# Performance work log

Hardware: AMD Instinct MI355X
Metric: run time of the kernel (lower is better)

## Reference

```python
import jax, jax.numpy as jnp
import numpy as np
from jax.ops import segment_sum, segment_max

DIM = 64; EDGE_DIM = 6; ACTION_DIM = 6
N = 16384; E = 32768; G = 256; TPG = 12  # nodes, edges, graphs, torsions/graph


def setup_inputs() -> dict:
    key = jax.random.key(0)
    ks = jax.random.split(key, 16)
    d = DIM
    def lin(k, fo, fi):
        return (jax.random.normal(k, (fo, fi), jnp.float32) / np.sqrt(fi)).astype(jnp.float32)
    return {
        "x": jax.random.normal(ks[0], (N, 3), jnp.float32),
        "edge_attr": jax.random.normal(ks[1], (E, EDGE_DIM), jnp.float32),
        "edge_index": jax.random.randint(ks[2], (2, E), 0, N),
        "batch": (jnp.arange(N) // (N // G)).astype(jnp.int32),
        "nonring": jax.random.randint(ks[3], (G * TPG, 4), 0, N),
        "nrbidx": (jnp.arange(G * TPG) // TPG).astype(jnp.int32),
        "num_graphs": G,
        "torsion_size": TPG,
        "lin0_w": lin(ks[4], d, 3), "lin0_b": jnp.zeros((d,), jnp.float32),
        "e1_w": lin(ks[5], d, EDGE_DIM), "e1_b": jnp.zeros((d,), jnp.float32),
        "e2_w": lin(ks[6], d * d, d), "e2_b": jnp.zeros((d * d,), jnp.float32),
        "root_w": lin(ks[7], d, d), "conv_b": jnp.zeros((d,), jnp.float32),
        "gru_wih": lin(ks[8], 3 * d, d), "gru_whh": lin(ks[9], 3 * d, d),
        "gru_bih": jnp.zeros((3 * d,), jnp.float32), "gru_bhh": jnp.zeros((3 * d,), jnp.float32),
        "s2s_wih": lin(ks[10], 4 * d, 2 * d), "s2s_whh": lin(ks[11], 4 * d, d),
        "s2s_bih": jnp.zeros((4 * d,), jnp.float32), "s2s_bhh": jnp.zeros((4 * d,), jnp.float32),
        "mem_wih": lin(ks[12], 4 * d, 2 * d), "mem_whh": lin(ks[13], 4 * d, d),
        "mem_bih": jnp.zeros((4 * d,), jnp.float32), "mem_bhh": jnp.zeros((4 * d,), jnp.float32),
        "lin1_w": lin(ks[14], d, 5 * d), "lin1_b": jnp.zeros((d,), jnp.float32),
        "lin2_w": lin(ks[15], ACTION_DIM, d), "lin2_b": jnp.zeros((ACTION_DIM,), jnp.float32),
    }


def _lstm_step(xin, h, c, wih, whh, bih, bhh):
    g = xin @ wih.T + bih + h @ whh.T + bhh
    i, f, gg, o = jnp.split(g, 4, axis=-1)
    c = jax.nn.sigmoid(f) * c + jax.nn.sigmoid(i) * jnp.tanh(gg)
    h = jax.nn.sigmoid(o) * jnp.tanh(c)
    return h, c


def _model(x, edge_attr, lin0_w, lin0_b, e1_w, e1_b, e2_w, e2_b, root_w, conv_b,
           gru_wih, gru_whh, gru_bih, gru_bhh, s2s_wih, s2s_whh, s2s_bih, s2s_bhh,
           mem_wih, mem_whh, mem_bih, mem_bhh, lin1_w, lin1_b, lin2_w, lin2_b,
           edge_index, batch, nonring, nrbidx, num_graphs, torsion_size):
    d = lin0_w.shape[0]
    n = x.shape[0]
    out = jax.nn.relu(x @ lin0_w.T + lin0_b)           # [N, d]
    h = out                                            # GRU hidden
    src, dst = edge_index[0], edge_index[1]
    # edge-conditioned weights (fixed across the 6 iterations -> computed once)
    ew = (jax.nn.relu(edge_attr @ e1_w.T + e1_b) @ e2_w.T + e2_b).reshape(-1, d, d)  # [E, d, d]
    deg = jnp.clip(segment_sum(jnp.ones((src.shape[0],), out.dtype), dst, num_segments=n), 1.0)
    for _ in range(6):
        msg = jnp.einsum('ei,eio->eo', out[src], ew)   # per-edge matmul, [E, d]
        agg = segment_sum(msg, dst, num_segments=n) / deg[:, None]  # scatter-mean
        m = jax.nn.relu(agg + out @ root_w + conv_b)
        gi = m @ gru_wih.T + gru_bih
        gh = h @ gru_whh.T + gru_bhh
        r = jax.nn.sigmoid(gi[:, :d] + gh[:, :d])
        z = jax.nn.sigmoid(gi[:, d:2 * d] + gh[:, d:2 * d])
        nnew = jnp.tanh(gi[:, 2 * d:] + r * gh[:, 2 * d:])
        h = (1.0 - z) * nnew + z * h
        out = h
    # Set2Set pooling, 6 processing steps
    q_star = jnp.zeros((num_graphs, 2 * d), out.dtype)
    hs = jnp.zeros((num_graphs, d), out.dtype); cs = jnp.zeros_like(hs)
    for _ in range(6):
        hs, cs = _lstm_step(q_star, hs, cs, s2s_wih, s2s_whh, s2s_bih, s2s_bhh)
        e = jnp.sum(out * hs[batch], axis=-1)
        emax = segment_max(e, batch, num_segments=num_graphs)
        a = jnp.exp(e - emax[batch])
        a = a / segment_sum(a, batch, num_segments=num_graphs)[batch]
        r_ = segment_sum(a[:, None] * out, batch, num_segments=num_graphs)
        q_star = jnp.concatenate([hs, r_], axis=-1)
    # memory LSTM, single step from zero state
    hx = jnp.zeros((num_graphs, d), out.dtype); cx = jnp.zeros_like(hx)
    hx, cx = _lstm_step(q_star, hx, cx, mem_wih, mem_whh, mem_bih, mem_bhh)
    lstm_sel = hx[nrbidx]                                   # [T, d]
    node_sel = out[nonring.reshape(-1)].reshape(4, -1, d)   # faithful to .view(4,-1,dim)
    stacked = jnp.concatenate([lstm_sel[None], node_sel], axis=0)  # [5, T, d]
    feat = jnp.transpose(stacked, (2, 1, 0)).reshape(-1, 5 * d)    # faithful permute+reshape -> [T, 5d]
    o1 = jax.nn.relu(feat @ lin1_w.T + lin1_b)
    logits = o1 @ lin2_w.T + lin2_b                          # [T, action_dim]
    logit = logits.reshape(num_graphs, torsion_size, -1)     # uniform split + pad_sequence
    return logit, hx[None], cx[None]


def reference(x, edge_attr, edge_index, batch, nonring, nrbidx, num_graphs, torsion_size,
              lin0_w, lin0_b, e1_w, e1_b, e2_w, e2_b, root_w, conv_b,
              gru_wih, gru_whh, gru_bih, gru_bhh, s2s_wih, s2s_whh, s2s_bih, s2s_bhh,
              mem_wih, mem_whh, mem_bih, mem_bhh, lin1_w, lin1_b, lin2_w, lin2_b):
    return _model(x, edge_attr, lin0_w, lin0_b, e1_w, e1_b, e2_w, e2_b, root_w, conv_b,
                  gru_wih, gru_whh, gru_bih, gru_bhh, s2s_wih, s2s_whh, s2s_bih, s2s_bhh,
                  mem_wih, mem_whh, mem_bih, mem_bhh, lin1_w, lin1_b, lin2_w, lin2_b,
                  edge_index, batch, nonring, nrbidx, num_graphs, torsion_size)
```

## Files before the change

kernel.cpp:

```cpp
#include <hip/hip_runtime.h>

#define NNODE 16384
#define NEDGE 32768
#define NG    256
#define TPGx  12
#define TTOT  (NG * TPGx)
#define D     64

typedef _Float16 h8 __attribute__((ext_vector_type(8)));
typedef float    f4 __attribute__((ext_vector_type(4)));

static __device__ __forceinline__ float sigm(float x) { return 1.f / (1.f + __expf(-x)); }

static __device__ __forceinline__ f4 mfma16h(h8 a, h8 b, f4 c) {
  return __builtin_amdgcn_mfma_f32_16x16x32_f16(a, b, c, 0, 0, 0);
}

static __device__ __forceinline__ h8 splat16(_Float16 x) {
  h8 v = {x, x, x, x, x, x, x, x};
  return v;
}

static __device__ __forceinline__ void gload_lds16(const void* g, void* l) {
  __builtin_amdgcn_global_load_lds(
      (const __attribute__((address_space(1))) unsigned int*)g,
      (__attribute__((address_space(3))) unsigned int*)l, 16, 0, 0);
}

#define WS_H      0
#define WS_AGG    4194304
#define WS_W2     8388608
#define WS_RT     8921088
#define WS_WHH    8929280
#define WS_WIH    8953856
#define WS_SWIHT  8978432
#define WS_SWHHT  9109504
#define WS_MWIHT  9175040
#define WS_L1WT   9306112
#define WS_L2WF   9388032
#define WS_FB     9389568
#define WS_DEG    9398784
#define WS_HX     9464320
#define WS_NEED   9529856

struct Srcs { const void* p[23]; };

__device__ __constant__ const int kCum[24] = {
    0, 192, 256, 640, 704, 262848, 266944, 271040, 271104, 283392, 295680,
    295872, 296064, 328832, 345216, 345472, 345728, 378496, 378752, 379008,
    399488, 399552, 399936, 399942};

__global__ __launch_bounds__(256) void pack_kernel(Srcs S, char* __restrict__ ws) {
  int idx = blockIdx.x * 256 + threadIdx.x;
  if (idx >= 399942) return;
  int r = 0, base = 0;
#pragma unroll
  for (int k = 0; k < 23; k++)
    if (idx >= kCum[k]) { r = k; base = kCum[k]; }
  int li = idx - base;
  float v = ((const float*)S.p[r])[li];

  float*    fb    = (float*)(ws + WS_FB);
  _Float16* w2    = (_Float16*)(ws + WS_W2);
  _Float16* rtH   = (_Float16*)(ws + WS_RT);
  _Float16* whhH  = (_Float16*)(ws + WS_WHH);
  _Float16* wihH  = (_Float16*)(ws + WS_WIH);
  float*    swihT = (float*)(ws + WS_SWIHT);
  float*    swhhT = (float*)(ws + WS_SWHHT);
  float*    mwihT = (float*)(ws + WS_MWIHT);
  float*    l1wT  = (float*)(ws + WS_L1WT);
  float*    l2w   = (float*)(ws + WS_L2WF);

  switch (r) {
    case 0: fb[li] = v; break;
    case 1: fb[192 + li] = v; break;
    case 2: fb[256 + li] = v; break;
    case 3: fb[640 + li] = v; break;
    case 4: {
      int i = li >> 12, o = (li >> 6) & 63, k = li & 63;
      w2[i * 4096 + (((k >> 3) * 64 + o) << 3) + (k & 7)] = (_Float16)v;
    } break;
    case 5: {
      int k = li >> 6, o = li & 63;
      w2[64 * 4096 + (((k >> 3) * 64 + o) << 3) + (k & 7)] = (_Float16)v;
    } break;
    case 6: {
      int i = li >> 6, o = li & 63;
      rtH[o * 64 + i] = (_Float16)v;
    } break;
    case 7: fb[704 + li] = v; break;
    case 8: wihH[li] = (_Float16)v; break;
    case 9: whhH[li] = (_Float16)v; break;
    case 10: fb[768 + li] = v; break;
    case 11: fb[960 + li] = v; break;
    case 12: swihT[(li & 127) * 256 + (li >> 7)] = v; break;
    case 13: swhhT[(li & 63) * 256 + (li >> 6)] = v; break;
    case 14: fb[1152 + li] = v; break;
    case 15: fb[1408 + li] = v; break;
    case 16: mwihT[(li & 127) * 256 + (li >> 7)] = v; break;
    case 17: fb[1664 + li] = v; break;
    case 18: fb[1920 + li] = v; break;
    case 19: l1wT[(li % 320) * 64 + (li / 320)] = v; break;
    case 20: fb[2176 + li] = v; break;
    case 21: l2w[li] = v; break;
    case 22: fb[2240 + li] = v; break;
  }
}

__global__ __launch_bounds__(256) void init_kernel(
    const float* __restrict__ x, const float* __restrict__ fb,
    float* __restrict__ h) {
  int idx = blockIdx.x * 256 + threadIdx.x;
  int n = idx >> 6, o = idx & 63;
  float acc = fb[192 + o];
#pragma unroll
  for (int j = 0; j < 3; j++) acc += x[n * 3 + j] * fb[o * 3 + j];
  h[idx] = fmaxf(acc, 0.f);
}

__global__ __launch_bounds__(256) void deg_kernel(const int* __restrict__ edge_index,
                                                  float* __restrict__ deg) {
  int e = blockIdx.x * 256 + threadIdx.x;
  if (e < NEDGE) atomicAdd(&deg[edge_index[NEDGE + e]], 1.0f);
}

__global__ __launch_bounds__(256) void msg_kernel(
    const float* __restrict__ h, const float* __restrict__ ea,
    const float* __restrict__ fb, const _Float16* __restrict__ w2,
    const int* __restrict__ edge_index, float* __restrict__ agg) {
  __shared__ _Float16 sOut[64][72];
  __shared__ _Float16 sB[2][16384];
  const int tid = threadIdx.x;
  const int wave = tid >> 6, lane = tid & 63;
  const int m15 = lane & 15, quad = lane >> 4;
  const int eg = wave >> 1;
  const int cg = wave & 1;
  const int eb = blockIdx.x * 64;
  {
    int r = tid >> 2, c0 = (tid & 3) * 16;
    int srcn = edge_index[eb + r];
#pragma unroll
    for (int c = c0; c < c0 + 16; c += 4) {
      float4 v = *(const float4*)&h[srcn * D + c];
      sOut[r][c]     = (_Float16)v.x;
      sOut[r][c + 1] = (_Float16)v.y;
      sOut[r][c + 2] = (_Float16)v.z;
      sOut[r][c + 3] = (_Float16)v.w;
    }
  }
  const int erowA = eg * 32 + m15;
  const int erowB = erowA + 16;
  const int e1 = eb + erowA, e2 = eb + erowB;
  h8 hidA0, hidA1, hidB0, hidB1;
  {
    float eav1[6], eav2[6];
#pragma unroll
    for (int j = 0; j < 6; j++) { eav1[j] = ea[e1 * 6 + j]; eav2[j] = ea[e2 * 6 + j]; }
#pragma unroll
    for (int j = 0; j < 8; j++) {
      int k0 = quad * 8 + j, k1 = 32 + quad * 8 + j;
      float a01 = fb[640 + k0], a11 = fb[640 + k1];
      float a02 = a01, a12 = a11;
#pragma unroll
      for (int jj = 0; jj < 6; jj++) {
        float w0 = fb[256 + k0 * 6 + jj], w1 = fb[256 + k1 * 6 + jj];
        a01 += eav1[jj] * w0; a11 += eav1[jj] * w1;
        a02 += eav2[jj] * w0; a12 += eav2[jj] * w1;
      }
      hidA0[j] = (_Float16)fmaxf(a01, 0.f);
      hidA1[j] = (_Float16)fmaxf(a11, 0.f);
      hidB0[j] = (_Float16)fmaxf(a02, 0.f);
      hidB1[j] = (_Float16)fmaxf(a12, 0.f);
    }
  }
  for (int c = wave; c < 32; c += 4)
    gload_lds16(w2 + c * 512 + lane * 8, &sB[0][c * 512]);
  __syncthreads();
  f4 zz = {0.f, 0.f, 0.f, 0.f};
  f4 accA[2], accB[2];
#pragma unroll
  for (int j = 0; j < 2; j++) { accA[j] = zz; accB[j] = zz; }
  for (int p = 0; p < 17; p++) {
    const int cur = p & 1;
    if (p < 16) {
      int nch = (p == 15) ? 8 : 32;
      const _Float16* src = w2 + (p + 1) * 16384;
      for (int c = wave; c < nch; c += 4)
        gload_lds16(src + c * 512 + lane * 8, &sB[cur ^ 1][c * 512]);
    }
    const int cnt = (p == 16) ? 1 : 4;
    for (int t = 0; t < cnt; t++) {
      const int i = p * 4 + t;
      h8 a10, a11, a20, a21;
      if (i < 64) {
        h8 o1 = splat16(sOut[erowA][i]);
        h8 o2 = splat16(sOut[erowB][i]);
        a10 = hidA0 * o1; a11 = hidA1 * o1;
        a20 = hidB0 * o2; a21 = hidB1 * o2;
      } else {
        a10 = *(const h8*)&sOut[erowA][quad * 8];
        a11 = *(const h8*)&sOut[erowA][32 + quad * 8];
        a20 = *(const h8*)&sOut[erowB][quad * 8];
        a21 = *(const h8*)&sOut[erowB][32 + quad * 8];
      }
      const _Float16* base = &sB[cur][t * 4096];
      const int q512 = quad * 512;
#pragma unroll
      for (int j = 0; j < 2; j++) {
        int nt = cg * 2 + j;
        int br8 = (nt * 16 + m15) * 8;
        h8 bh0 = *(const h8*)(base + q512 + br8);
        h8 bh1 = *(const h8*)(base + 2048 + q512 + br8);
        accA[j] = mfma16h(a10, bh0, accA[j]);
        accA[j] = mfma16h(a11, bh1, accA[j]);
        accB[j] = mfma16h(a20, bh0, accB[j]);
        accB[j] = mfma16h(a21, bh1, accB[j]);
      }
    }
    __syncthreads();
  }
#pragma unroll
  for (int reg = 0; reg < 4; reg++) {
    int rA = eb + eg * 32 + quad * 4 + reg;
    int rB = rA + 16;
    int dnA = edge_index[NEDGE + rA];
    int dnB = edge_index[NEDGE + rB];
#pragma unroll
    for (int j = 0; j < 2; j++) {
      int o = (cg * 2 + j) * 16 + m15;
      atomicAdd(agg + dnA * D + o, accA[j][reg]);
      atomicAdd(agg + dnB * D + o, accB[j][reg]);
    }
  }
}

__global__ __launch_bounds__(256) void update_kernel(
    float* __restrict__ h, float* __restrict__ agg, const float* __restrict__ deg,
    const _Float16* __restrict__ rtH, const _Float16* __restrict__ whhH,
    const _Float16* __restrict__ wihH, const float* __restrict__ fb) {
  __shared__ float buf[64][68];
  const int tid = threadIdx.x;
  const int wave = tid >> 6, lane = tid & 63;
  const int m15 = lane & 15, quad = lane >> 4;
  const int nb = blockIdx.x * 64;
  {
    int r = tid >> 2, c0 = (tid & 3) * 16;
#pragma unroll
    for (int c = c0; c < c0 + 16; c += 4)
      *(float4*)&buf[r][c] = *(const float4*)&h[(nb + r) * D + c];
  }
  __syncthreads();
  const int mrow = wave * 16 + m15;
  h8 a0, a1;
#pragma unroll
  for (int j = 0; j < 8; j++) {
    a0[j] = (_Float16)buf[mrow][quad * 8 + j];
    a1[j] = (_Float16)buf[mrow][32 + quad * 8 + j];
  }
  f4 zz = {0.f, 0.f, 0.f, 0.f};
  f4 acc[16];
#pragma unroll
  for (int nt = 0; nt < 16; nt++) acc[nt] = zz;
#pragma unroll
  for (int nt = 0; nt < 16; nt++) {
    int nn = nt * 16 + m15;
    const _Float16* bp = (nt < 4) ? (rtH + nn * D) : (whhH + (nn - 64) * D);
    h8 bh0 = *(const h8*)(bp + quad * 8);
    h8 bh1 = *(const h8*)(bp + 32 + quad * 8);
    f4 a = acc[nt];
    a = mfma16h(a0, bh0, a);
    a = mfma16h(a1, bh1, a);
    acc[nt] = a;
  }
  __syncthreads();
#pragma unroll
  for (int nt = 0; nt < 4; nt++) {
#pragma unroll
    for (int reg = 0; reg < 4; reg++) {
      int nloc = wave * 16 + quad * 4 + reg;
      int o = nt * 16 + m15;
      float dg = fmaxf(deg[nb + nloc], 1.f);
      int aidx = (nb + nloc) * D + o;
      float v = acc[nt][reg] + agg[aidx] / dg + fb[704 + o];
      agg[aidx] = 0.f;
      buf[nloc][o] = fmaxf(v, 0.f);
    }
  }
  __syncthreads();
  h8 m0, m1;
#pragma unroll
  for (int j = 0; j < 8; j++) {
    m0[j] = (_Float16)buf[mrow][quad * 8 + j];
    m1[j] = (_Float16)buf[mrow][32 + quad * 8 + j];
  }
  f4 g2[12];
#pragma unroll
  for (int nt = 0; nt < 12; nt++) g2[nt] = zz;
#pragma unroll
  for (int nt = 0; nt < 12; nt++) {
    int nn = nt * 16 + m15;
    const _Float16* bp = wihH + nn * D;
    h8 bh0 = *(const h8*)(bp + quad * 8);
    h8 bh1 = *(const h8*)(bp + 32 + quad * 8);
    f4 a = g2[nt];
    a = mfma16h(m0, bh0, a);
    a = mfma16h(m1, bh1, a);
    g2[nt] = a;
  }
#pragma unroll
  for (int nt = 0; nt < 4; nt++) {
#pragma unroll
    for (int reg = 0; reg < 4; reg++) {
      int nloc = wave * 16 + quad * 4 + reg;
      int o = nt * 16 + m15;
      int gidx = (nb + nloc) * D + o;
      float gir = g2[nt][reg]      + fb[768 + o];
      float giz = g2[nt + 4][reg]  + fb[768 + 64 + o];
      float gin = g2[nt + 8][reg]  + fb[768 + 128 + o];
      float ghr = acc[nt + 4][reg]  + fb[960 + o];
      float ghz = acc[nt + 8][reg]  + fb[960 + 64 + o];
      float ghn = acc[nt + 12][reg] + fb[960 + 128 + o];
      float rr = sigm(gir + ghr);
      float zg = sigm(giz + ghz);
      float nnv = tanhf(gin + rr * ghn);
      float hv = h[gidx];
      h[gidx] = (1.f - zg) * nnv + zg * hv;
    }
  }
}

__global__ __launch_bounds__(256) void s2s_kernel(
    const float* __restrict__ h,
    const float* __restrict__ wihT, const float* __restrict__ whhT,
    const float* __restrict__ mwihT, const float* __restrict__ fb,
    float* __restrict__ hx_f32, float* __restrict__ dout) {
  __shared__ float outL[64][65];
  __shared__ float qs[128];
  __shared__ float hsv[64], csv[64], sg[256], sa[64];
  __shared__ float spart[4][64];
  const int t = threadIdx.x;
  const int g = blockIdx.x;
  for (int idx = t; idx < 64 * 64; idx += 256) outL[idx >> 6][idx & 63] = h[g * 4096 + idx];
  if (t < 128) qs[t] = 0.f;
  if (t < 64) { hsv[t] = 0.f; csv[t] = 0.f; }
  __syncthreads();
  for (int step = 0; step < 6; step++) {
    float acc = fb[1152 + t] + fb[1408 + t];
#pragma unroll 8
    for (int j = 0; j < 128; j++) acc += qs[j] * wihT[j * 256 + t];
#pragma unroll 8
    for (int j = 0; j < 64; j++) acc += hsv[j] * whhT[j * 256 + t];
    sg[t] = acc;
    __syncthreads();
    if (t < 64) {
      float cn = sigm(sg[64 + t]) * csv[t] + sigm(sg[t]) * tanhf(sg[128 + t]);
      csv[t] = cn;
      hsv[t] = sigm(sg[192 + t]) * tanhf(cn);
    }
    __syncthreads();
    if (t < 64) {
      float e = 0.f;
      for (int d2 = 0; d2 < 64; d2++) e += outL[t][d2] * hsv[d2];
      float mx = e;
      for (int off = 32; off > 0; off >>= 1) mx = fmaxf(mx, __shfl_xor(mx, off));
      float a = __expf(e - mx);
      float s = a;
      for (int off = 32; off > 0; off >>= 1) s += __shfl_xor(s, off);
      sa[t] = a / s;
    }
    __syncthreads();
    {
      int o = t & 63, part = t >> 6;
      float r = 0.f;
      for (int n2 = part * 16; n2 < part * 16 + 16; n2++) r += sa[n2] * outL[n2][o];
      spart[part][o] = r;
    }
    __syncthreads();
    if (t < 64) {
      qs[t] = hsv[t];
      qs[64 + t] = spart[0][t] + spart[1][t] + spart[2][t] + spart[3][t];
    }
    __syncthreads();
  }
  float acc = fb[1664 + t] + fb[1920 + t];
#pragma unroll 8
  for (int j = 0; j < 128; j++) acc += qs[j] * mwihT[j * 256 + t];
  sg[t] = acc;
  __syncthreads();
  if (t < 64) {
    float cn = sigm(sg[t]) * tanhf(sg[128 + t]);
    float hn = sigm(sg[192 + t]) * tanhf(cn);
    hx_f32[g * 64 + t] = hn;
    dout[TTOT * 6 + g * 64 + t] = hn;
    dout[TTOT * 6 + NG * 64 + g * 64 + t] = cn;
  }
}

__global__ __launch_bounds__(64) void head_kernel(
    const float* __restrict__ h, const float* __restrict__ hx_f32,
    const int* __restrict__ nonring, const int* __restrict__ nrbidx,
    const float* __restrict__ l1wT, const float* __restrict__ l2w,
    const float* __restrict__ fb, float* __restrict__ dout) {
  __shared__ float feat[320];
  __shared__ float so1[64];
  const int r = blockIdx.x;
  const int lane = threadIdx.x;
  const int blk = r % 48, di = r / 48;
  const int tt = blk * 64 + lane;
  feat[lane * 5] = hx_f32[nrbidx[tt] * 64 + di];
#pragma unroll
  for (int s = 1; s <= 4; s++)
    feat[lane * 5 + s] = h[nonring[(s - 1) * TTOT + tt] * 64 + di];
  __syncthreads();
  float acc = fb[2176 + lane];
#pragma unroll 8
  for (int c = 0; c < 320; c++) acc += feat[c] * l1wT[c * 64 + lane];
  so1[lane] = fmaxf(acc, 0.f);
  __syncthreads();
  if (lane < 6) {
    float a2 = fb[2240 + lane];
    for (int j = 0; j < 64; j++) a2 += so1[j] * l2w[lane * 64 + j];
    dout[r * 6 + lane] = a2;
  }
}

extern "C" void kernel_launch(void* const* d_in, const int* in_sizes, int n_in,
                              void* d_out, int out_size, void* d_ws, size_t ws_size,
                              hipStream_t stream) {
  (void)in_sizes; (void)n_in; (void)out_size;
  const float* x         = (const float*)d_in[0];
  const float* edge_attr = (const float*)d_in[1];
  const int* edge_index  = (const int*)d_in[2];
  const int* nonring     = (const int*)d_in[4];
  const int* nrbidx      = (const int*)d_in[5];
  float* out = (float*)d_out;

  char* ws = (char*)d_ws;
  float*    h      = (float*)(ws + WS_H);
  float*    agg    = (float*)(ws + WS_AGG);
  _Float16* w2     = (_Float16*)(ws + WS_W2);
  _Float16* rtH    = (_Float16*)(ws + WS_RT);
  _Float16* whhH   = (_Float16*)(ws + WS_WHH);
  _Float16* wihH   = (_Float16*)(ws + WS_WIH);
  float*    swihT  = (float*)(ws + WS_SWIHT);
  float*    swhhT  = (float*)(ws + WS_SWHHT);
  float*    mwihT  = (float*)(ws + WS_MWIHT);
  float*    l1wT   = (float*)(ws + WS_L1WT);
  float*    l2wF   = (float*)(ws + WS_L2WF);
  float*    fb     = (float*)(ws + WS_FB);
  float*    deg    = (float*)(ws + WS_DEG);
  float*    hx_f32 = (float*)(ws + WS_HX);
  if (ws_size < (size_t)WS_NEED) return;

  Srcs S;
  S.p[0] = d_in[8];   S.p[1] = d_in[9];   S.p[2] = d_in[10];  S.p[3] = d_in[11];
  S.p[4] = d_in[12];  S.p[5] = d_in[13];  S.p[6] = d_in[14];  S.p[7] = d_in[15];
  S.p[8] = d_in[16];  S.p[9] = d_in[17];  S.p[10] = d_in[18]; S.p[11] = d_in[19];
  S.p[12] = d_in[20]; S.p[13] = d_in[21]; S.p[14] = d_in[22]; S.p[15] = d_in[23];
  S.p[16] = d_in[24]; S.p[17] = d_in[26]; S.p[18] = d_in[27]; S.p[19] = d_in[28];
  S.p[20] = d_in[29]; S.p[21] = d_in[30]; S.p[22] = d_in[31];
  pack_kernel<<<(399942 + 255) / 256, 256, 0, stream>>>(S, ws);

  init_kernel<<<NNODE * D / 256, 256, 0, stream>>>(x, fb, h);
  hipMemsetAsync(deg, 0, NNODE * 4, stream);
  hipMemsetAsync(agg, 0, NNODE * D * 4, stream);
  deg_kernel<<<NEDGE / 256, 256, 0, stream>>>(edge_index, deg);

  for (int it = 0; it < 6; it++) {
    msg_kernel<<<NEDGE / 64, 256, 0, stream>>>(h, edge_attr, fb, w2, edge_index, agg);
    update_kernel<<<NNODE / 64, 256, 0, stream>>>(h, agg, deg, rtH, whhH, wihH, fb);
  }

  s2s_kernel<<<NG, 256, 0, stream>>>(h, swihT, swhhT, mwihT, fb, hx_f32, out);
  head_kernel<<<TTOT, 64, 0, stream>>>(h, hx_f32, nonring, nrbidx, l1wT, l2wF, fb, out);
}
```

Baseline: 498.6 us.

## Stream edge-network weights from global into registers and cache s2s weights

The message kernel drops its double-buffered LDS staging of the 64x64x64 edge-network weights. Each wave now owns a 16-column output slice across all 64 edges and loads its weight fragments straight from global memory into registers, prefetching one stage ahead, so the per-stage block barriers go away. Each wave also now computes four edge-row tiles instead of two. Separately, the set2set kernel keeps its 128 input-weight values per thread in registers across the six LSTM steps instead of reloading them every step. The risks are higher register pressure and global/L2 traffic for weights that were previously shared through LDS.

After: 443.4 us (median of 2 runs). -11.1%, faster.

```diff
diff --git a/kernel.cpp b/kernel.cpp
--- a/kernel.cpp
+++ b/kernel.cpp
@@ -8,6 +8,7 @@
 #define D     64
 
 typedef _Float16 h8 __attribute__((ext_vector_type(8)));
+typedef _Float16 h4 __attribute__((ext_vector_type(4)));
 typedef float    f4 __attribute__((ext_vector_type(4)));
 
 static __device__ __forceinline__ float sigm(float x) { return 1.f / (1.f + __expf(-x)); }
@@ -19,12 +20,6 @@
 static __device__ __forceinline__ h8 splat16(_Float16 x) {
   h8 v = {x, x, x, x, x, x, x, x};
   return v;
-}
-
-static __device__ __forceinline__ void gload_lds16(const void* g, void* l) {
-  __builtin_amdgcn_global_load_lds(
-      (const __attribute__((address_space(1))) unsigned int*)g,
-      (__attribute__((address_space(3))) unsigned int*)l, 16, 0, 0);
 }
 
 #define WS_H      0
@@ -129,12 +124,9 @@
     const float* __restrict__ fb, const _Float16* __restrict__ w2,
     const int* __restrict__ edge_index, float* __restrict__ agg) {
   __shared__ _Float16 sOut[64][72];
-  __shared__ _Float16 sB[2][16384];
   const int tid = threadIdx.x;
   const int wave = tid >> 6, lane = tid & 63;
   const int m15 = lane & 15, quad = lane >> 4;
-  const int eg = wave >> 1;
-  const int cg = wave & 1;
   const int eb = blockIdx.x * 64;
   {
     int r = tid >> 2, c0 = (tid & 3) * 16;
@@ -148,88 +140,83 @@
       sOut[r][c + 3] = (_Float16)v.w;
     }
   }
-  const int erowA = eg * 32 + m15;
-  const int erowB = erowA + 16;
-  const int e1 = eb + erowA, e2 = eb + erowB;
-  h8 hidA0, hidA1, hidB0, hidB1;
-  {
-    float eav1[6], eav2[6];
-#pragma unroll
-    for (int j = 0; j < 6; j++) { eav1[j] = ea[e1 * 6 + j]; eav2[j] = ea[e2 * 6 + j]; }
+  h8 hid0[4], hid1[4];
+#pragma unroll
+  for (int r = 0; r < 4; r++) {
+    int e = eb + r * 16 + m15;
+    float eav[6];
+#pragma unroll
+    for (int j = 0; j < 6; j++) eav[j] = ea[e * 6 + j];
 #pragma unroll
     for (int j = 0; j < 8; j++) {
       int k0 = quad * 8 + j, k1 = 32 + quad * 8 + j;
-      float a01 = fb[640 + k0], a11 = fb[640 + k1];
-      float a02 = a01, a12 = a11;
+      float a0 = fb[640 + k0], a1 = fb[640 + k1];
 #pragma unroll
       for (int jj = 0; jj < 6; jj++) {
-        float w0 = fb[256 + k0 * 6 + jj], w1 = fb[256 + k1 * 6 + jj];
-        a01 += eav1[jj] * w0; a11 += eav1[jj] * w1;
-        a02 += eav2[jj] * w0; a12 += eav2[jj] * w1;
+        a0 += eav[jj] * fb[256 + k0 * 6 + jj];
+        a1 += eav[jj] * fb[256 + k1 * 6 + jj];
       }
-      hidA0[j] = (_Float16)fmaxf(a01, 0.f);
-      hidA1[j] = (_Float16)fmaxf(a11, 0.f);
-      hidB0[j] = (_Float16)fmaxf(a02, 0.f);
-      hidB1[j] = (_Float16)fmaxf(a12, 0.f);
-    }
-  }
-  for (int c = wave; c < 32; c += 4)
-    gload_lds16(w2 + c * 512 + lane * 8, &sB[0][c * 512]);
-  __syncthreads();
+      hid0[r][j] = (_Float16)fmaxf(a0, 0.f);
+      hid1[r][j] = (_Float16)fmaxf(a1, 0.f);
+    }
+  }
+  __syncthreads();
+  const _Float16* bp0 = w2 + (quad * 64 + wave * 16 + m15) * 8;
+  const _Float16* bp1 = w2 + ((4 + quad) * 64 + wave * 16 + m15) * 8;
   f4 zz = {0.f, 0.f, 0.f, 0.f};
-  f4 accA[2], accB[2];
-#pragma unroll
-  for (int j = 0; j < 2; j++) { accA[j] = zz; accB[j] = zz; }
-  for (int p = 0; p < 17; p++) {
-    const int cur = p & 1;
-    if (p < 16) {
-      int nch = (p == 15) ? 8 : 32;
-      const _Float16* src = w2 + (p + 1) * 16384;
-      for (int c = wave; c < nch; c += 4)
-        gload_lds16(src + c * 512 + lane * 8, &sB[cur ^ 1][c * 512]);
-    }
-    const int cnt = (p == 16) ? 1 : 4;
-    for (int t = 0; t < cnt; t++) {
-      const int i = p * 4 + t;
-      h8 a10, a11, a20, a21;
-      if (i < 64) {
-        h8 o1 = splat16(sOut[erowA][i]);
-        h8 o2 = splat16(sOut[erowB][i]);
-        a10 = hidA0 * o1; a11 = hidA1 * o1;
-        a20 = hidB0 * o2; a21 = hidB1 * o2;
-      } else {
-        a10 = *(const h8*)&sOut[erowA][quad * 8];
-        a11 = *(const h8*)&sOut[erowA][32 + quad * 8];
-        a20 = *(const h8*)&sOut[erowB][quad * 8];
-        a21 = *(const h8*)&sOut[erowB][32 + quad * 8];
+  f4 acc[4];
+#pragma unroll
+  for (int r = 0; r < 4; r++) acc[r] = zz;
+  h8 c0[4], c1[4];
+#pragma unroll
+  for (int t = 0; t < 4; t++) {
+    c0[t] = *(const h8*)(bp0 + t * 4096);
+    c1[t] = *(const h8*)(bp1 + t * 4096);
+  }
+#pragma unroll
+  for (int p = 0; p < 16; p++) {
+    h8 n0[4], n1[4];
+    if (p < 15) {
+#pragma unroll
+      for (int t = 0; t < 4; t++) {
+        int i = (p + 1) * 4 + t;
+        n0[t] = *(const h8*)(bp0 + i * 4096);
+        n1[t] = *(const h8*)(bp1 + i * 4096);
       }
-      const _Float16* base = &sB[cur][t * 4096];
-      const int q512 = quad * 512;
-#pragma unroll
-      for (int j = 0; j < 2; j++) {
-        int nt = cg * 2 + j;
-        int br8 = (nt * 16 + m15) * 8;
-        h8 bh0 = *(const h8*)(base + q512 + br8);
-        h8 bh1 = *(const h8*)(base + 2048 + q512 + br8);
-        accA[j] = mfma16h(a10, bh0, accA[j]);
-        accA[j] = mfma16h(a11, bh1, accA[j]);
-        accB[j] = mfma16h(a20, bh0, accB[j]);
-        accB[j] = mfma16h(a21, bh1, accB[j]);
+    }
+#pragma unroll
+    for (int r = 0; r < 4; r++) {
+      h4 os4 = *(const h4*)&sOut[r * 16 + m15][p * 4];
+#pragma unroll
+      for (int t = 0; t < 4; t++) {
+        h8 os = splat16(os4[t]);
+        acc[r] = mfma16h(hid0[r] * os, c0[t], acc[r]);
+        acc[r] = mfma16h(hid1[r] * os, c1[t], acc[r]);
       }
     }
-    __syncthreads();
-  }
-#pragma unroll
-  for (int reg = 0; reg < 4; reg++) {
-    int rA = eb + eg * 32 + quad * 4 + reg;
-    int rB = rA + 16;
-    int dnA = edge_index[NEDGE + rA];
-    int dnB = edge_index[NEDGE + rB];
-#pragma unroll
-    for (int j = 0; j < 2; j++) {
-      int o = (cg * 2 + j) * 16 + m15;
-      atomicAdd(agg + dnA * D + o, accA[j][reg]);
-      atomicAdd(agg + dnB * D + o, accB[j][reg]);
+    if (p < 15) {
+#pragma unroll
+      for (int t = 0; t < 4; t++) { c0[t] = n0[t]; c1[t] = n1[t]; }
+    }
+  }
+  {
+    h8 b0 = *(const h8*)(bp0 + 64 * 4096);
+    h8 b1 = *(const h8*)(bp1 + 64 * 4096);
+#pragma unroll
+    for (int r = 0; r < 4; r++) {
+      h8 a0 = *(const h8*)&sOut[r * 16 + m15][quad * 8];
+      h8 a1 = *(const h8*)&sOut[r * 16 + m15][32 + quad * 8];
+      acc[r] = mfma16h(a0, b0, acc[r]);
+      acc[r] = mfma16h(a1, b1, acc[r]);
+    }
+  }
+#pragma unroll
+  for (int r = 0; r < 4; r++) {
+#pragma unroll
+    for (int reg = 0; reg < 4; reg++) {
+      int ee = eb + r * 16 + quad * 4 + reg;
+      int dn = edge_index[NEDGE + ee];
+      atomicAdd(agg + dn * D + wave * 16 + m15, acc[r][reg]);
     }
   }
 }
@@ -340,14 +327,17 @@
   __shared__ float spart[4][64];
   const int t = threadIdx.x;
   const int g = blockIdx.x;
+  float wr[128];
+#pragma unroll
+  for (int j = 0; j < 128; j++) wr[j] = wihT[j * 256 + t];
   for (int idx = t; idx < 64 * 64; idx += 256) outL[idx >> 6][idx & 63] = h[g * 4096 + idx];
   if (t < 128) qs[t] = 0.f;
   if (t < 64) { hsv[t] = 0.f; csv[t] = 0.f; }
   __syncthreads();
   for (int step = 0; step < 6; step++) {
     float acc = fb[1152 + t] + fb[1408 + t];
-#pragma unroll 8
-    for (int j = 0; j < 128; j++) acc += qs[j] * wihT[j * 256 + t];
+#pragma unroll
+    for (int j = 0; j < 128; j++) acc += qs[j] * wr[j];
 #pragma unroll 8
     for (int j = 0; j < 64; j++) acc += hsv[j] * whhT[j * 256 + t];
     sg[t] = acc;
```
